# Optimization experiments

Measured on AMD Instinct MI355X. Metric: run time of the kernel, lower is better.

## Reference

```python
import jax, jax.numpy as jnp
import numpy as np
from jax import lax

B, N, S = 4, 16384, 4096
D1, D2 = 128, 256
MLP = (256, 128)
EPS_W = 1e-8
EPS_BN = 1e-5
BIG = 1e8


def setup_inputs() -> dict:
    key = jax.random.key(0)
    ks = jax.random.split(key, 10)
    inp = {
        "xyz1": jax.random.normal(ks[0], (B, 3, N), jnp.float32),
        "xyz2": jax.random.normal(ks[1], (B, 3, S), jnp.float32),
        "points1": jax.random.normal(ks[2], (B, D1, N), jnp.float32),
        "points2": jax.random.normal(ks[3], (B, D2, S), jnp.float32),
        "idx1": jnp.repeat(jnp.arange(B, dtype=jnp.int32), N).reshape(B, N),
        "idx2": jnp.repeat(jnp.arange(B, dtype=jnp.int32), S).reshape(B, S),
    }
    cin = D1 + D2
    inp["w1"] = jax.random.normal(ks[4], (MLP[0], cin), jnp.float32) * 0.05
    inp["b1"] = jnp.zeros((MLP[0],), jnp.float32)
    inp["g1"] = jnp.ones((MLP[0],), jnp.float32)
    inp["be1"] = jnp.zeros((MLP[0],), jnp.float32)
    inp["w2"] = jax.random.normal(ks[5], (MLP[1], MLP[0]), jnp.float32) * 0.05
    inp["b2"] = jnp.zeros((MLP[1],), jnp.float32)
    inp["g2"] = jnp.ones((MLP[1],), jnp.float32)
    inp["be2"] = jnp.zeros((MLP[1],), jnp.float32)
    return inp


def _bn_relu(x, gamma, beta):
    # training-mode batchnorm over (B, N) per channel, then relu; x: [B, C, N]
    mean = jnp.mean(x, axis=(0, 2), keepdims=True)
    var = jnp.var(x, axis=(0, 2), keepdims=True)  # biased, as torch BN
    xn = (x - mean) * lax.rsqrt(var + EPS_BN)
    return jax.nn.relu(xn * gamma[None, :, None] + beta[None, :, None])


def _fp_forward(xyz1, xyz2, points1, points2, idx1, idx2,
                w1, b1, g1, be1, w2, b2, g2, be2):
    x1 = jnp.transpose(xyz1, (0, 2, 1))  # [B, N, 3]
    x2 = jnp.transpose(xyz2, (0, 2, 1))  # [B, S, 3]
    p2 = jnp.transpose(points2, (0, 2, 1))  # [B, S, D2]

    # squared pairwise distances [B, N, S]
    d = -2.0 * jnp.einsum('bnc,bsc->bns', x1, x2)
    d = d + jnp.sum(x1 * x1, -1)[:, :, None] + jnp.sum(x2 * x2, -1)[:, None, :]
    d = jnp.where(idx1[:, :, None] == idx2[:, None, :], d, jnp.inf)

    # 3 nearest neighbors (top-k on negated distances == sort-ascending take 3)
    neg_d3, idx3 = lax.top_k(-d, 3)          # [B, N, 3]
    d3 = -neg_d3
    recip = 1.0 / (d3 + EPS_W)
    weight = recip / jnp.sum(recip, axis=2, keepdims=True)
    weight = jnp.where(d3 > BIG, 0.0, weight)
    weight = jnp.nan_to_num(weight)

    gathered = jax.vmap(lambda p, i: p[i])(p2, idx3)   # [B, N, 3, D2]
    interp = jnp.sum(gathered * weight[..., None], axis=2)  # [B, N, D2]

    newp = jnp.concatenate([jnp.transpose(points1, (0, 2, 1)), interp], axis=-1)
    newp = jnp.transpose(newp, (0, 2, 1))  # [B, D1+D2, N]

    # 1x1 conv -> BN -> relu, twice
    h = jnp.einsum('bcn,oc->bon', newp, w1) + b1[None, :, None]
    h = _bn_relu(h, g1, be1)
    h = jnp.einsum('bcn,oc->bon', h, w2) + b2[None, :, None]
    h = _bn_relu(h, g2, be2)
    return h


def reference(xyz1, xyz2, points1, points2, idx1, idx2,
              w1, b1, g1, be1, w2, b2, g2, be2):
    return _fp_forward(xyz1, xyz2, points1, points2, idx1, idx2,
                       w1, b1, g1, be1, w2, b2, g2, be2)
```

## Files before the change

kernel.cpp:

```cpp
#include <hip/hip_runtime.h>
#include <hip/hip_bf16.h>

#define INF_F (__builtin_inff())

typedef __attribute__((ext_vector_type(8))) short bf16x8;
typedef __attribute__((ext_vector_type(4))) float f32x4;

__device__ __forceinline__ unsigned short f2bf(float f) {
  __hip_bfloat16 h = __float2bfloat16(f);
  return __builtin_bit_cast(unsigned short, h);
}
__device__ __forceinline__ float bf2f(unsigned short u) {
  return __uint_as_float((unsigned)u << 16);
}

#define TOP3_INS(d, sj, E0, E1, E2, J0, J1, J2)                      \
  {                                                                  \
    bool l0 = (d) < E0, l1 = (d) < E1;                               \
    E2 = l1 ? E1 : (d); J2 = l1 ? J1 : (sj);                         \
    E1 = l0 ? E0 : (l1 ? (d) : E1); J1 = l0 ? J0 : (l1 ? (sj) : J1); \
    E0 = l0 ? (d) : E0; J0 = l0 ? (sj) : J0;                         \
  }


__global__ __launch_bounds__(256) void prep_k(const float* __restrict__ p2,
                                              const float* __restrict__ p1,
                                              const float* __restrict__ w1,
                                              const float* __restrict__ w2,
                                              const float* __restrict__ xyz2,
                                              const int* __restrict__ idx1,
                                              const int* __restrict__ idx2,
                                              unsigned short* __restrict__ p2t,
                                              unsigned short* __restrict__ X,
                                              unsigned short* __restrict__ w1b,
                                              unsigned short* __restrict__ w2b,
                                              float4* __restrict__ pack) {
  int id = blockIdx.x;
  int t = threadIdx.x;
  if (id < 4096) {
    __shared__ float tile[32][33];
    int s0 = (id & 127) * 32;
    int k0 = ((id >> 7) & 7) * 32;
    int b = id >> 10;
    int tx = t & 31, ty = t >> 5;
    const float* src = p2 + ((size_t)b * 256 + k0) * 4096 + s0;
    for (int r = ty; r < 32; r += 8) tile[r][tx] = src[(size_t)r * 4096 + tx];
    __syncthreads();
    unsigned short* dst = p2t + ((size_t)b * 4096 + s0) * 256 + k0;
    for (int r = ty; r < 32; r += 8) dst[(size_t)r * 256 + tx] = f2bf(tile[tx][r]);
  } else if (id < 12288) {
    __shared__ float tile[32][33];
    int id2 = id - 4096;
    int n0 = (id2 & 511) * 32;
    int c0 = ((id2 >> 9) & 3) * 32;
    int b = id2 >> 11;
    int tx = t & 31, ty = t >> 5;
    const float* src = p1 + ((size_t)b * 128 + c0) * 16384 + n0;
    for (int r = ty; r < 32; r += 8) tile[r][tx] = src[(size_t)r * 16384 + tx];
    __syncthreads();
    for (int r = ty; r < 32; r += 8)
      X[((size_t)(b * 16384 + n0 + r)) * 384 + c0 + tx] = f2bf(tile[tx][r]);
  } else {
    int id3 = (id - 12288) * 256 + t;
    if (id3 < 98304) {
      w1b[id3] = f2bf(w1[id3]);
    } else if (id3 < 131072) {
      w2b[id3 - 98304] = f2bf(w2[id3 - 98304]);
    } else {
      int pid = id3 - 131072;
      int b = pid >> 12, s = pid & 4095;
      float x = xyz2[(b * 3 + 0) * 4096 + s];
      float y = xyz2[(b * 3 + 1) * 4096 + s];
      float z = xyz2[(b * 3 + 2) * 4096 + s];
      float w = fmaf(x, x, fmaf(y, y, z * z));
      int common = idx1[b * 16384];
      w = (idx2[b * 4096 + s] == common) ? w : 3e38f;
      pack[b * 4096 + s] = make_float4(x, y, z, w);
    }
  }
}

__global__ __launch_bounds__(256) void knn_k(const float* __restrict__ xyz1,
                                             const float* __restrict__ xyz2,
                                             const int* __restrict__ idx1,
                                             const int* __restrict__ idx2,
                                             const float4* __restrict__ pack,
                                             float* __restrict__ rec) {
  int bid = blockIdx.x;
  int qg = bid >> 3, sl = bid & 7;
  int b = qg >> 6;
  int nloc = (qg & 63) << 8;
  int t = threadIdx.x;
  int n = nloc + t;
  int q0i = b * 16384 + n;
  int common = idx1[b * 16384];
  int sbase = sl << 9;
  const float4* ps = pack + b * 4096 + sbase;
  float px = xyz1[(b * 3 + 0) * 16384 + n];
  float py = xyz1[(b * 3 + 1) * 16384 + n];
  float pz = xyz1[(b * 3 + 2) * 16384 + n];
  int myid = idx1[q0i];
  float pn = fmaf(px, px, fmaf(py, py, pz * pz));
  float qx = -2.f * px, qy = -2.f * py, qz = -2.f * pz;
  float e0 = INF_F, e1 = INF_F, e2 = INF_F;
  int j0 = 0, j1 = 0, j2 = 0;
#pragma unroll 8
  for (int s = 0; s < 512; ++s) {
    float4 p = ps[s];
    float d = fmaf(qx, p.x, fmaf(qy, p.y, fmaf(qz, p.z, pn))) + p.w;
    if (__builtin_expect(d < e2, 0)) {
      int sj = sbase + s;
      TOP3_INS(d, sj, e0, e1, e2, j0, j1, j2);
    }
  }
  if (__builtin_expect(myid != common, 0)) {
    e0 = INF_F; e1 = INF_F; e2 = INF_F; j0 = 0; j1 = 0; j2 = 0;
    for (int s = 0; s < 512; ++s) {
      int gs = sbase + s;
      float x = xyz2[(b * 3 + 0) * 4096 + gs];
      float y = xyz2[(b * 3 + 1) * 4096 + gs];
      float z = xyz2[(b * 3 + 2) * 4096 + gs];
      float w = fmaf(x, x, fmaf(y, y, z * z));
      float d = fmaf(qx, x, fmaf(qy, y, fmaf(qz, z, pn))) + w;
      d = (idx2[b * 4096 + gs] == myid) ? d : INF_F;
      if (d < e2) TOP3_INS(d, gs, e0, e1, e2, j0, j1, j2);
    }
  }
  float* r = &rec[((size_t)sl * 65536 + q0i) * 6];
  r[0] = e0; r[1] = e1; r[2] = e2;
  ((int*)r)[3] = j0; ((int*)r)[4] = j1; ((int*)r)[5] = j2;
}

__global__ __launch_bounds__(256) void interpm_k(const float* __restrict__ rec,
                                                 const unsigned short* __restrict__ p2t,
                                                 unsigned short* __restrict__ X) {
  __shared__ int sId[128][3];
  __shared__ float sWt[128][3];
  int i0 = blockIdx.x * 128;
  int b = i0 >> 14;
  int t = threadIdx.x;
  if (t < 128) {
    int i = i0 + t;
    float e0, e1, e2;
    int j0, j1, j2;
    {
      const float* r = &rec[(size_t)i * 6];
      e0 = r[0]; e1 = r[1]; e2 = r[2];
      j0 = ((const int*)r)[3]; j1 = ((const int*)r)[4]; j2 = ((const int*)r)[5];
    }
#pragma unroll
    for (int c = 1; c < 8; ++c) {
      const float* r = &rec[((size_t)c * 65536 + i) * 6];
      const int* ir = (const int*)r;
#pragma unroll
      for (int w = 0; w < 3; ++w) {
        float d = r[w];
        int sj = ir[3 + w];
        bool l0 = (d < e0) || (d == e0 && sj < j0);
        bool l1 = (d < e1) || (d == e1 && sj < j1);
        bool l2 = (d < e2) || (d == e2 && sj < j2);
        e2 = l1 ? e1 : (l2 ? d : e2);
        j2 = l1 ? j1 : (l2 ? sj : j2);
        e1 = l0 ? e0 : (l1 ? d : e1);
        j1 = l0 ? j0 : (l1 ? sj : j1);
        e0 = l0 ? d : e0;
        j0 = l0 ? sj : j0;
      }
    }
    float r0 = 1.f / (e0 + 1e-8f);
    float r1 = 1.f / (e1 + 1e-8f);
    float r2 = 1.f / (e2 + 1e-8f);
    float rs = r0 + r1 + r2;
    sWt[t][0] = (e0 > 1e8f) ? 0.f : r0 / rs;
    sWt[t][1] = (e1 > 1e8f) ? 0.f : r1 / rs;
    sWt[t][2] = (e2 > 1e8f) ? 0.f : r2 / rs;
    sId[t][0] = j0; sId[t][1] = j1; sId[t][2] = j2;
  }
  __syncthreads();
  int k = t;
  const unsigned short* base = p2t + (size_t)b * 4096 * 256;
#pragma unroll 2
  for (int ii = 0; ii < 128; ++ii) {
    int id0 = sId[ii][0], id1 = sId[ii][1], id2 = sId[ii][2];
    float w0 = sWt[ii][0], w1v = sWt[ii][1], w2v = sWt[ii][2];
    float v = w0 * bf2f(base[id0 * 256 + k]);
    v = fmaf(w1v, bf2f(base[id1 * 256 + k]), v);
    v = fmaf(w2v, bf2f(base[id2 * 256 + k]), v);
    X[(size_t)(i0 + ii) * 384 + 128 + k] = f2bf(v);
  }
}

__global__ __launch_bounds__(256) void gemm1_k(const unsigned short* __restrict__ X,
                                               const unsigned short* __restrict__ Wb,
                                               unsigned short* __restrict__ h1T,
                                               float* __restrict__ part1) {
  __shared__ unsigned short sW[128][40];
  __shared__ unsigned short sX[128][40];
  int t = threadIdx.x;
  int i0 = blockIdx.x * 128;
  int c0 = blockIdx.y * 128;
  int w = t >> 6, lane = t & 63;
  int wc = (w & 1) * 64, wni = w >> 1;
  int wn = wni * 64;
  int l15 = lane & 15, g = lane >> 4;
  f32x4 acc[4][4];
#pragma unroll
  for (int a = 0; a < 4; ++a)
#pragma unroll
    for (int bq = 0; bq < 4; ++bq) acc[a][bq] = (f32x4)0.f;
  int sr = t & 127, sh = t >> 7;
  for (int kc = 0; kc < 12; ++kc) {
    int k0 = kc * 32;
    __syncthreads();
    {
      const uint4* gw = (const uint4*)&Wb[(size_t)(c0 + sr) * 384 + k0 + sh * 16];
      uint4 v0 = gw[0], v1 = gw[1];
      *(uint4*)&sW[sr][sh * 16] = v0;
      *(uint4*)&sW[sr][sh * 16 + 8] = v1;
      const uint4* gx = (const uint4*)&X[(size_t)(i0 + sr) * 384 + k0 + sh * 16];
      uint4 x0 = gx[0], x1 = gx[1];
      *(uint4*)&sX[sr][sh * 16] = x0;
      *(uint4*)&sX[sr][sh * 16 + 8] = x1;
    }
    __syncthreads();
    bf16x8 a[4], b[4];
#pragma unroll
    for (int tm = 0; tm < 4; ++tm)
      a[tm] = *(const bf16x8*)&sW[wc + tm * 16 + l15][g * 8];
#pragma unroll
    for (int tn = 0; tn < 4; ++tn)
      b[tn] = *(const bf16x8*)&sX[wn + tn * 16 + l15][g * 8];
#pragma unroll
    for (int tm = 0; tm < 4; ++tm)
#pragma unroll
      for (int tn = 0; tn < 4; ++tn)
        acc[tm][tn] = __builtin_amdgcn_mfma_f32_16x16x32_bf16(a[tm], b[tn], acc[tm][tn], 0, 0, 0);
  }
#pragma unroll
  for (int tm = 0; tm < 4; ++tm)
#pragma unroll
    for (int tn = 0; tn < 4; ++tn) {
      int c = c0 + wc + tm * 16 + g * 4;
      int n = i0 + wn + tn * 16 + l15;
      f32x4 v = acc[tm][tn];
      ushort4 o;
      o.x = f2bf(v[0]); o.y = f2bf(v[1]); o.z = f2bf(v[2]); o.w = f2bf(v[3]);
      *(ushort4*)&h1T[(size_t)n * 256 + c] = o;
    }
  float s_[4][4], q_[4][4];
#pragma unroll
  for (int tm = 0; tm < 4; ++tm)
#pragma unroll
    for (int j = 0; j < 4; ++j) {
      float s = 0.f, q = 0.f;
#pragma unroll
      for (int tn = 0; tn < 4; ++tn) {
        float v = acc[tm][tn][j];
        s += v; q = fmaf(v, v, q);
      }
      s_[tm][j] = s; q_[tm][j] = q;
    }
#pragma unroll
  for (int mask = 1; mask < 16; mask <<= 1)
#pragma unroll
    for (int tm = 0; tm < 4; ++tm)
#pragma unroll
      for (int j = 0; j < 4; ++j) {
        s_[tm][j] += __shfl_xor(s_[tm][j], mask);
        q_[tm][j] += __shfl_xor(q_[tm][j], mask);
      }
  __syncthreads();
  float* red = (float*)&sW[0][0];
  if (l15 == 0) {
#pragma unroll
    for (int tm = 0; tm < 4; ++tm)
#pragma unroll
      for (int j = 0; j < 4; ++j) {
        int cl = wc + tm * 16 + g * 4 + j;
        red[(wni * 128 + cl) * 2 + 0] = s_[tm][j];
        red[(wni * 128 + cl) * 2 + 1] = q_[tm][j];
      }
  }
  __syncthreads();
  if (t < 256) {
    int cl = t >> 1, st = t & 1;
    float v = red[(0 * 128 + cl) * 2 + st] + red[(1 * 128 + cl) * 2 + st];
    part1[((size_t)blockIdx.x * 256 + c0 + cl) * 2 + st] = v;
  }
}

template <int C, int NB>
__global__ __launch_bounds__(256) void bnfold_k(const float* __restrict__ part,
                                                const float* __restrict__ g,
                                                const float* __restrict__ be,
                                                float* __restrict__ A,
                                                float* __restrict__ Cc) {
  int c = threadIdx.x;
  if (c >= C) return;
  float s1 = 0.f, s2 = 0.f;
  for (int b = 0; b < NB; ++b) {
    s1 += part[((size_t)b * C + c) * 2 + 0];
    s2 += part[((size_t)b * C + c) * 2 + 1];
  }
  float mean = s1 * (1.f / 65536.f);
  float var = s2 * (1.f / 65536.f) - mean * mean;
  float a = g[c] * rsqrtf(var + 1e-5f);
  A[c] = a;
  Cc[c] = be[c] - mean * a;
}

__global__ __launch_bounds__(256) void gemm2_k(const unsigned short* __restrict__ h1T,
                                               const unsigned short* __restrict__ Wb,
                                               const float* __restrict__ A,
                                               const float* __restrict__ C,
                                               float* __restrict__ o2,
                                               float* __restrict__ part2) {
  __shared__ unsigned short sW[128][40];
  __shared__ unsigned short sX[128][40];
  int t = threadIdx.x;
  int i0 = blockIdx.x * 128;
  int w = t >> 6, lane = t & 63;
  int wc = (w & 1) * 64, wni = w >> 1;
  int wn = wni * 64;
  int l15 = lane & 15, g = lane >> 4;
  f32x4 acc[4][4];
#pragma unroll
  for (int a = 0; a < 4; ++a)
#pragma unroll
    for (int bq = 0; bq < 4; ++bq) acc[a][bq] = (f32x4)0.f;
  int sr = t & 127, sh = t >> 7;
  for (int kc = 0; kc < 8; ++kc) {
    int k0 = kc * 32;
    int kcol = k0 + sh * 16;
    __syncthreads();
    {
      const uint4* gw = (const uint4*)&Wb[(size_t)sr * 256 + kcol];
      uint4 v0 = gw[0], v1 = gw[1];
      *(uint4*)&sW[sr][sh * 16] = v0;
      *(uint4*)&sW[sr][sh * 16 + 8] = v1;
      const uint4* gx = (const uint4*)&h1T[(size_t)(i0 + sr) * 256 + kcol];
      uint4 x0 = gx[0], x1 = gx[1];
      unsigned rr[8] = {x0.x, x0.y, x0.z, x0.w, x1.x, x1.y, x1.z, x1.w};
      unsigned ww[8];
#pragma unroll
      for (int e = 0; e < 8; ++e) {
        int ch = kcol + 2 * e;
        float f0 = bf2f((unsigned short)(rr[e] & 0xFFFFu));
        float f1 = bf2f((unsigned short)(rr[e] >> 16));
        f0 = fmaxf(fmaf(A[ch], f0, C[ch]), 0.f);
        f1 = fmaxf(fmaf(A[ch + 1], f1, C[ch + 1]), 0.f);
        ww[e] = (unsigned)f2bf(f0) | ((unsigned)f2bf(f1) << 16);
      }
      uint4 y0 = {ww[0], ww[1], ww[2], ww[3]};
      uint4 y1 = {ww[4], ww[5], ww[6], ww[7]};
      *(uint4*)&sX[sr][sh * 16] = y0;
      *(uint4*)&sX[sr][sh * 16 + 8] = y1;
    }
    __syncthreads();
    bf16x8 a[4], b[4];
#pragma unroll
    for (int tm = 0; tm < 4; ++tm)
      a[tm] = *(const bf16x8*)&sW[wc + tm * 16 + l15][g * 8];
#pragma unroll
    for (int tn = 0; tn < 4; ++tn)
      b[tn] = *(const bf16x8*)&sX[wn + tn * 16 + l15][g * 8];
#pragma unroll
    for (int tm = 0; tm < 4; ++tm)
#pragma unroll
      for (int tn = 0; tn < 4; ++tn)
        acc[tm][tn] = __builtin_amdgcn_mfma_f32_16x16x32_bf16(a[tm], b[tn], acc[tm][tn], 0, 0, 0);
  }
#pragma unroll
  for (int tm = 0; tm < 4; ++tm)
#pragma unroll
    for (int tn = 0; tn < 4; ++tn) {
      int c = wc + tm * 16 + g * 4;
      int n = i0 + wn + tn * 16 + l15;
      f32x4 v = acc[tm][tn];
      *(float4*)&o2[(size_t)n * 128 + c] = make_float4(v[0], v[1], v[2], v[3]);
    }
  float s_[4][4], q_[4][4];
#pragma unroll
  for (int tm = 0; tm < 4; ++tm)
#pragma unroll
    for (int j = 0; j < 4; ++j) {
      float s = 0.f, q = 0.f;
#pragma unroll
      for (int tn = 0; tn < 4; ++tn) {
        float v = acc[tm][tn][j];
        s += v; q = fmaf(v, v, q);
      }
      s_[tm][j] = s; q_[tm][j] = q;
    }
#pragma unroll
  for (int mask = 1; mask < 16; mask <<= 1)
#pragma unroll
    for (int tm = 0; tm < 4; ++tm)
#pragma unroll
      for (int j = 0; j < 4; ++j) {
        s_[tm][j] += __shfl_xor(s_[tm][j], mask);
        q_[tm][j] += __shfl_xor(q_[tm][j], mask);
      }
  __syncthreads();
  float* red = (float*)&sW[0][0];
  if (l15 == 0) {
#pragma unroll
    for (int tm = 0; tm < 4; ++tm)
#pragma unroll
      for (int j = 0; j < 4; ++j) {
        int cl = wc + tm * 16 + g * 4 + j;
        red[(wni * 128 + cl) * 2 + 0] = s_[tm][j];
        red[(wni * 128 + cl) * 2 + 1] = q_[tm][j];
      }
  }
  __syncthreads();
  if (t < 256) {
    int cl = t >> 1, st = t & 1;
    float v = red[(0 * 128 + cl) * 2 + st] + red[(1 * 128 + cl) * 2 + st];
    part2[((size_t)blockIdx.x * 128 + cl) * 2 + st] = v;
  }
}

__global__ __launch_bounds__(256) void final_k(const float* __restrict__ o2,
                                               const float* __restrict__ A,
                                               const float* __restrict__ C,
                                               float* __restrict__ out) {
  __shared__ float tile[32][33];
  int b = blockIdx.z;
  int n0 = blockIdx.x * 32;
  int c0 = blockIdx.y * 32;
  int tx = threadIdx.x, ty = threadIdx.y;
  float a = A[c0 + tx], cc = C[c0 + tx];
  for (int r = ty; r < 32; r += 8) {
    float v = o2[(size_t)(b * 16384 + n0 + r) * 128 + c0 + tx];
    tile[r][tx] = fmaxf(fmaf(a, v, cc), 0.f);
  }
  __syncthreads();
  for (int r = ty; r < 32; r += 8)
    out[((size_t)(b * 128 + c0 + r)) * 16384 + n0 + tx] = tile[tx][r];
}

extern "C" void kernel_launch(void* const* d_in, const int* in_sizes, int n_in,
                              void* d_out, int out_size, void* d_ws, size_t ws_size,
                              hipStream_t stream) {
  const float* xyz1 = (const float*)d_in[0];
  const float* xyz2 = (const float*)d_in[1];
  const float* p1   = (const float*)d_in[2];
  const float* p2   = (const float*)d_in[3];
  const int*   idx1 = (const int*)d_in[4];
  const int*   idx2 = (const int*)d_in[5];
  const float* w1   = (const float*)d_in[6];
  const float* g1   = (const float*)d_in[8];
  const float* be1  = (const float*)d_in[9];
  const float* w2   = (const float*)d_in[10];
  const float* g2   = (const float*)d_in[12];
  const float* be2  = (const float*)d_in[13];
  float* out = (float*)d_out;

  char* ws = (char*)d_ws;
  unsigned short* X    = (unsigned short*)(ws + 0x180000);
  unsigned short* h1T  = (unsigned short*)(ws + 0x3180000);
  unsigned short* p2t  = (unsigned short*)(ws + 0x3180000);
  float*          o2   = (float*)(ws + 0x5180000);
  float*          rec  = (float*)(ws + 0x5180000);
  unsigned short* w1b  = (unsigned short*)(ws + 0x7180000);
  unsigned short* w2b  = (unsigned short*)(ws + 0x71B0000);
  float*          part1 = (float*)(ws + 0x71C0000);
  float*          part2 = (float*)(ws + 0x72C0000);
  float4*         pack = (float4*)(ws + 0x7340000);
  float*          a1   = (float*)(ws + 0x7388000);
  float*          c1   = a1 + 256;
  float*          a2   = c1 + 256;
  float*          c2   = a2 + 128;

  hipLaunchKernelGGL(prep_k, dim3(12864), dim3(256), 0, stream,
                     p2, p1, w1, w2, xyz2, idx1, idx2, p2t, X, w1b, w2b, pack);
  hipLaunchKernelGGL(knn_k, dim3(2048), dim3(256), 0, stream,
                     xyz1, xyz2, idx1, idx2, pack, rec);
  hipLaunchKernelGGL(interpm_k, dim3(512), dim3(256), 0, stream, rec, p2t, X);
  hipLaunchKernelGGL(gemm1_k, dim3(512, 2), dim3(256), 0, stream, X, w1b, h1T, part1);
  hipLaunchKernelGGL((bnfold_k<256, 512>), dim3(1), dim3(256), 0, stream,
                     part1, g1, be1, a1, c1);
  hipLaunchKernelGGL(gemm2_k, dim3(512), dim3(256), 0, stream,
                     h1T, w2b, a1, c1, o2, part2);
  hipLaunchKernelGGL((bnfold_k<128, 512>), dim3(1), dim3(256), 0, stream,
                     part2, g2, be2, a2, c2);
  hipLaunchKernelGGL(final_k, dim3(512, 4, 4), dim3(32, 8), 0, stream, o2, a2, c2, out);
}
```

Before: 249.6 us.

## Replace BN fold kernels with atomic stats and store gemm2 output in bf16

Per-block BN partial sums are now accumulated with atomicAdd into a small stats buffer that prep_k zeroes. This removes the two single-block bnfold kernels and their launches. The BN scale and shift are recomputed per block in gemm2 and final_k from those stats. Separately, the gemm2 output o2 is stored as bf16 instead of fp32, halving that intermediate's traffic at some cost in precision. Atomic accumulation makes the summation order nondeterministic, and there are 512–1024 contending atomics per address.

```diff
diff --git a/kernel.cpp b/kernel.cpp
--- a/kernel.cpp
+++ b/kernel.cpp
@@ -34,7 +34,8 @@
                                               unsigned short* __restrict__ X,
                                               unsigned short* __restrict__ w1b,
                                               unsigned short* __restrict__ w2b,
-                                              float4* __restrict__ pack) {
+                                              float4* __restrict__ pack,
+                                              float* __restrict__ stats) {
   int id = blockIdx.x;
   int t = threadIdx.x;
   if (id < 4096) {
@@ -60,7 +61,7 @@
     __syncthreads();
     for (int r = ty; r < 32; r += 8)
       X[((size_t)(b * 16384 + n0 + r)) * 384 + c0 + tx] = f2bf(tile[tx][r]);
-  } else {
+  } else if (id < 12864) {
     int id3 = (id - 12288) * 256 + t;
     if (id3 < 98304) {
       w1b[id3] = f2bf(w1[id3]);
@@ -77,6 +78,8 @@
       w = (idx2[b * 4096 + s] == common) ? w : 3e38f;
       pack[b * 4096 + s] = make_float4(x, y, z, w);
     }
+  } else {
+    for (int i = t; i < 768; i += 256) stats[i] = 0.f;
   }
 }
 
@@ -193,7 +196,7 @@
 __global__ __launch_bounds__(256) void gemm1_k(const unsigned short* __restrict__ X,
                                                const unsigned short* __restrict__ Wb,
                                                unsigned short* __restrict__ h1T,
-                                               float* __restrict__ part1) {
+                                               float* __restrict__ stats1) {
   __shared__ unsigned short sW[128][40];
   __shared__ unsigned short sX[128][40];
   int t = threadIdx.x;
@@ -282,47 +285,37 @@
       }
   }
   __syncthreads();
-  if (t < 256) {
+  {
     int cl = t >> 1, st = t & 1;
     float v = red[(0 * 128 + cl) * 2 + st] + red[(1 * 128 + cl) * 2 + st];
-    part1[((size_t)blockIdx.x * 256 + c0 + cl) * 2 + st] = v;
-  }
-}
-
-template <int C, int NB>
-__global__ __launch_bounds__(256) void bnfold_k(const float* __restrict__ part,
-                                                const float* __restrict__ g,
-                                                const float* __restrict__ be,
-                                                float* __restrict__ A,
-                                                float* __restrict__ Cc) {
-  int c = threadIdx.x;
-  if (c >= C) return;
-  float s1 = 0.f, s2 = 0.f;
-  for (int b = 0; b < NB; ++b) {
-    s1 += part[((size_t)b * C + c) * 2 + 0];
-    s2 += part[((size_t)b * C + c) * 2 + 1];
-  }
-  float mean = s1 * (1.f / 65536.f);
-  float var = s2 * (1.f / 65536.f) - mean * mean;
-  float a = g[c] * rsqrtf(var + 1e-5f);
-  A[c] = a;
-  Cc[c] = be[c] - mean * a;
+    atomicAdd(&stats1[((c0 + cl) << 1) + st], v);
+  }
 }
 
 __global__ __launch_bounds__(256) void gemm2_k(const unsigned short* __restrict__ h1T,
                                                const unsigned short* __restrict__ Wb,
-                                               const float* __restrict__ A,
-                                               const float* __restrict__ C,
-                                               float* __restrict__ o2,
-                                               float* __restrict__ part2) {
+                                               const float* __restrict__ stats1,
+                                               const float* __restrict__ g1,
+                                               const float* __restrict__ be1,
+                                               unsigned short* __restrict__ o2,
+                                               float* __restrict__ stats2) {
   __shared__ unsigned short sW[128][40];
   __shared__ unsigned short sX[128][40];
+  __shared__ float sA1[256], sC1[256];
   int t = threadIdx.x;
   int i0 = blockIdx.x * 128;
   int w = t >> 6, lane = t & 63;
   int wc = (w & 1) * 64, wni = w >> 1;
   int wn = wni * 64;
   int l15 = lane & 15, g = lane >> 4;
+  {
+    float s1v = stats1[t * 2 + 0], s2v = stats1[t * 2 + 1];
+    float mean = s1v * (1.f / 65536.f);
+    float var = s2v * (1.f / 65536.f) - mean * mean;
+    float a = g1[t] * rsqrtf(var + 1e-5f);
+    sA1[t] = a;
+    sC1[t] = be1[t] - mean * a;
+  }
   f32x4 acc[4][4];
 #pragma unroll
   for (int a = 0; a < 4; ++a)
@@ -347,8 +340,8 @@
         int ch = kcol + 2 * e;
         float f0 = bf2f((unsigned short)(rr[e] & 0xFFFFu));
         float f1 = bf2f((unsigned short)(rr[e] >> 16));
-        f0 = fmaxf(fmaf(A[ch], f0, C[ch]), 0.f);
-        f1 = fmaxf(fmaf(A[ch + 1], f1, C[ch + 1]), 0.f);
+        f0 = fmaxf(fmaf(sA1[ch], f0, sC1[ch]), 0.f);
+        f1 = fmaxf(fmaf(sA1[ch + 1], f1, sC1[ch + 1]), 0.f);
         ww[e] = (unsigned)f2bf(f0) | ((unsigned)f2bf(f1) << 16);
       }
       uint4 y0 = {ww[0], ww[1], ww[2], ww[3]};
@@ -377,7 +370,9 @@
       int c = wc + tm * 16 + g * 4;
       int n = i0 + wn + tn * 16 + l15;
       f32x4 v = acc[tm][tn];
-      *(float4*)&o2[(size_t)n * 128 + c] = make_float4(v[0], v[1], v[2], v[3]);
+      ushort4 o;
+      o.x = f2bf(v[0]); o.y = f2bf(v[1]); o.z = f2bf(v[2]); o.w = f2bf(v[3]);
+      *(ushort4*)&o2[(size_t)n * 128 + c] = o;
     }
   float s_[4][4], q_[4][4];
 #pragma unroll
@@ -414,25 +409,37 @@
       }
   }
   __syncthreads();
-  if (t < 256) {
+  {
     int cl = t >> 1, st = t & 1;
     float v = red[(0 * 128 + cl) * 2 + st] + red[(1 * 128 + cl) * 2 + st];
-    part2[((size_t)blockIdx.x * 128 + cl) * 2 + st] = v;
-  }
-}
-
-__global__ __launch_bounds__(256) void final_k(const float* __restrict__ o2,
-                                               const float* __restrict__ A,
-                                               const float* __restrict__ C,
+    atomicAdd(&stats2[(cl << 1) + st], v);
+  }
+}
+
+__global__ __launch_bounds__(256) void final_k(const unsigned short* __restrict__ o2,
+                                               const float* __restrict__ stats2,
+                                               const float* __restrict__ g2,
+                                               const float* __restrict__ be2,
                                                float* __restrict__ out) {
   __shared__ float tile[32][33];
+  __shared__ float sA2[128], sC2[128];
   int b = blockIdx.z;
   int n0 = blockIdx.x * 32;
   int c0 = blockIdx.y * 32;
   int tx = threadIdx.x, ty = threadIdx.y;
-  float a = A[c0 + tx], cc = C[c0 + tx];
+  int tid = ty * 32 + tx;
+  if (tid < 128) {
+    float s1v = stats2[tid * 2 + 0], s2v = stats2[tid * 2 + 1];
+    float mean = s1v * (1.f / 65536.f);
+    float var = s2v * (1.f / 65536.f) - mean * mean;
+    float a = g2[tid] * rsqrtf(var + 1e-5f);
+    sA2[tid] = a;
+    sC2[tid] = be2[tid] - mean * a;
+  }
+  __syncthreads();
+  float a = sA2[c0 + tx], cc = sC2[c0 + tx];
   for (int r = ty; r < 32; r += 8) {
-    float v = o2[(size_t)(b * 16384 + n0 + r) * 128 + c0 + tx];
+    float v = bf2f(o2[(size_t)(b * 16384 + n0 + r) * 128 + c0 + tx]);
     tile[r][tx] = fmaxf(fmaf(a, v, cc), 0.f);
   }
   __syncthreads();
@@ -461,29 +468,23 @@
   unsigned short* X    = (unsigned short*)(ws + 0x180000);
   unsigned short* h1T  = (unsigned short*)(ws + 0x3180000);
   unsigned short* p2t  = (unsigned short*)(ws + 0x3180000);
-  float*          o2   = (float*)(ws + 0x5180000);
+  unsigned short* o2   = (unsigned short*)(ws + 0x5180000);
   float*          rec  = (float*)(ws + 0x5180000);
   unsigned short* w1b  = (unsigned short*)(ws + 0x7180000);
   unsigned short* w2b  = (unsigned short*)(ws + 0x71B0000);
-  float*          part1 = (float*)(ws + 0x71C0000);
-  float*          part2 = (float*)(ws + 0x72C0000);
-  float4*         pack = (float4*)(ws + 0x7340000);
-  float*          a1   = (float*)(ws + 0x7388000);
-  float*          c1   = a1 + 256;
-  float*          a2   = c1 + 256;
-  float*          c2   = a2 + 128;
-
-  hipLaunchKernelGGL(prep_k, dim3(12864), dim3(256), 0, stream,
-                     p2, p1, w1, w2, xyz2, idx1, idx2, p2t, X, w1b, w2b, pack);
+  float4*         pack = (float4*)(ws + 0x71C0000);
+  float*          stats = (float*)(ws + 0x7208000);
+  float*          stats1 = stats;
+  float*          stats2 = stats + 512;
+
+  hipLaunchKernelGGL(prep_k, dim3(12865), dim3(256), 0, stream,
+                     p2, p1, w1, w2, xyz2, idx1, idx2, p2t, X, w1b, w2b, pack, stats);
   hipLaunchKernelGGL(knn_k, dim3(2048), dim3(256), 0, stream,
                      xyz1, xyz2, idx1, idx2, pack, rec);
   hipLaunchKernelGGL(interpm_k, dim3(512), dim3(256), 0, stream, rec, p2t, X);
-  hipLaunchKernelGGL(gemm1_k, dim3(512, 2), dim3(256), 0, stream, X, w1b, h1T, part1);
-  hipLaunchKernelGGL((bnfold_k<256, 512>), dim3(1), dim3(256), 0, stream,
-                     part1, g1, be1, a1, c1);
+  hipLaunchKernelGGL(gemm1_k, dim3(512, 2), dim3(256), 0, stream, X, w1b, h1T, stats1);
   hipLaunchKernelGGL(gemm2_k, dim3(512), dim3(256), 0, stream,
-                     h1T, w2b, a1, c1, o2, part2);
-  hipLaunchKernelGGL((bnfold_k<128, 512>), dim3(1), dim3(256), 0, stream,
-                     part2, g2, be2, a2, c2);
-  hipLaunchKernelGGL(final_k, dim3(512, 4, 4), dim3(32, 8), 0, stream, o2, a2, c2, out);
-}
+                     h1T, w2b, stats1, g1, be1, o2, stats2);
+  hipLaunchKernelGGL(final_k, dim3(512, 4, 4), dim3(32, 8), 0, stream,
+                     o2, stats2, g2, be2, out);
+}
```

Result: faster. 233.7 us (-6.4%).
